# Kernel optimization log

Measured on AMD Instinct MI355X. Metric: run time of the kernel, lower is better.

## Reference

```python
import jax, jax.numpy as jnp
import numpy as np

V = 100000   # input_size == output_size (item vocab)
H = 256      # hidden_size
B = 512      # batch_size
L = 1        # num_layers


def setup_inputs() -> dict:
    key = jax.random.key(0)
    k0, k1, k2, k3, k4 = jax.random.split(key, 5)
    s = 1.0 / np.sqrt(H)  # pytorch default uniform bound scale
    return {
        "input": jax.random.randint(k0, (B,), 0, V),
        "target": jax.random.randint(k1, (B,), 0, V),
        "hidden": jnp.zeros((L, B, H), jnp.float32),
        # GRU weights, pytorch gate layout [r; z; n]
        "w_ih": jax.random.uniform(k2, (3 * H, V), jnp.float32, -s, s),
        "w_hh": jax.random.uniform(k3, (3 * H, H), jnp.float32, -s, s),
        "b_ih": jnp.zeros((3 * H,), jnp.float32),
        "b_hh": jnp.zeros((3 * H,), jnp.float32),
        # h2o linear
        "w_out": jax.random.uniform(k4, (V, H), jnp.float32, -s, s),
        "b_out": jnp.zeros((V,), jnp.float32),
    }


def reference(input, target, hidden, w_ih, w_hh, b_ih, b_hh, w_out, b_out):
    # one-hot(input) @ w_ih.T is mathematically a column gather of w_ih
    h = hidden[0]                                        # (B, H)
    gi = jnp.take(w_ih, input, axis=1).T + b_ih          # (B, 3H)
    gh = h @ w_hh.T + b_hh                               # (B, 3H)
    i_r, i_z, i_n = jnp.split(gi, 3, axis=1)
    h_r, h_z, h_n = jnp.split(gh, 3, axis=1)
    r = jax.nn.sigmoid(i_r + h_r)
    z = jax.nn.sigmoid(i_z + h_z)
    n = jnp.tanh(i_n + r * h_n)
    h_new = (1.0 - z) * n + z * h                        # (B, H)
    logit = jnp.tanh(h_new @ w_out.T + b_out)            # (B, V)
    return logit, h_new[None]                            # ((B,V), (L,B,H))
```

## Files before the change

kernel.cpp:

```cpp
#include <hip/hip_runtime.h>
#include <hip/hip_bf16.h>
#include <math.h>

#define V 100000
#define H 256
#define B 512

typedef __bf16 bf16x8 __attribute__((ext_vector_type(8)));
typedef float  f32x4  __attribute__((ext_vector_type(4)));

__device__ __forceinline__ unsigned short f32_bf16_rne(float x) {
    unsigned u = __float_as_uint(x);
    u += 0x7FFFu + ((u >> 16) & 1u);
    return (unsigned short)(u >> 16);
}
__device__ __forceinline__ float bf16u_f32(unsigned short h) {
    return __uint_as_float(((unsigned)h) << 16);
}
__device__ __forceinline__ float fast_tanh(float x) {
    float e = __builtin_exp2f(x * 2.8853900817779268f);
    return 1.f - 2.f * __builtin_amdgcn_rcpf(e + 1.f);
}

#define GLOAD_LDS16(g, l)                                                     \
    __builtin_amdgcn_global_load_lds(                                         \
        (const __attribute__((address_space(1))) void*)(g),                   \
        (__attribute__((address_space(3))) void*)(l), 16, 0, 0)

__global__ __launch_bounds__(256) void split_w_kernel(
    const float*    __restrict__ w,
    unsigned short* __restrict__ hi,
    unsigned short* __restrict__ lo)
{
    const int total4 = (V * H) / 4;
    for (int i = blockIdx.x * blockDim.x + threadIdx.x; i < total4;
         i += gridDim.x * blockDim.x) {
        const float4 x = reinterpret_cast<const float4*>(w)[i];
        const float f[4] = {x.x, x.y, x.z, x.w};
        ushort4 hv, lv;
        unsigned short* hp = &hv.x;
        unsigned short* lp = &lv.x;
        #pragma unroll
        for (int j = 0; j < 4; ++j) {
            hp[j] = f32_bf16_rne(f[j]);
            lp[j] = f32_bf16_rne(f[j] - bf16u_f32(hp[j]));
        }
        reinterpret_cast<ushort4*>(hi)[i] = hv;
        reinterpret_cast<ushort4*>(lo)[i] = lv;
    }
}

__global__ __launch_bounds__(256) void gru_cell_kernel(
    const int*   __restrict__ input,
    const float* __restrict__ hidden,
    const float* __restrict__ w_ih,
    const float* __restrict__ w_hh,
    const float* __restrict__ b_ih,
    const float* __restrict__ b_hh,
    float*       __restrict__ h_out,
    unsigned short* __restrict__ h_hi_p,
    unsigned short* __restrict__ h_lo_p)
{
    const int b = blockIdx.x;
    const int j = threadIdx.x;

    __shared__ float hs[H];
    hs[j] = hidden[b * H + j];
    __syncthreads();

    const int idx = input[b];
    float gi_r = w_ih[ j          * V + idx] + b_ih[j];
    float gi_z = w_ih[(j +     H) * V + idx] + b_ih[j + H];
    float gi_n = w_ih[(j + 2 * H) * V + idx] + b_ih[j + 2 * H];

    const float4* wr = reinterpret_cast<const float4*>(&w_hh[ j          * H]);
    const float4* wz = reinterpret_cast<const float4*>(&w_hh[(j +     H) * H]);
    const float4* wn = reinterpret_cast<const float4*>(&w_hh[(j + 2 * H) * H]);
    const float4* h4 = reinterpret_cast<const float4*>(hs);

    float ar = 0.f, az = 0.f, an = 0.f;
    #pragma unroll 8
    for (int k = 0; k < H / 4; ++k) {
        const float4 hv = h4[k];
        const float4 a  = wr[k];
        const float4 c  = wz[k];
        const float4 d  = wn[k];
        ar += a.x * hv.x + a.y * hv.y + a.z * hv.z + a.w * hv.w;
        az += c.x * hv.x + c.y * hv.y + c.z * hv.z + c.w * hv.w;
        an += d.x * hv.x + d.y * hv.y + d.z * hv.z + d.w * hv.w;
    }

    const float h_r = ar + b_hh[j];
    const float h_z = az + b_hh[j + H];
    const float h_n = an + b_hh[j + 2 * H];

    const float r = 1.f / (1.f + expf(-(gi_r + h_r)));
    const float z = 1.f / (1.f + expf(-(gi_z + h_z)));
    const float n = tanhf(gi_n + r * h_n);
    const float hprev = hs[j];

    const float val = (1.f - z) * n + z * hprev;
    h_out[b * H + j] = val;
    if (h_hi_p != nullptr) {
        const unsigned short hh = f32_bf16_rne(val);
        h_hi_p[b * H + j] = hh;
        h_lo_p[b * H + j] = f32_bf16_rne(val - bf16u_f32(hh));
    }
}

#define BM  64
#define BN  128
#define BK  64
#define NVB 782
#define NBB 8

__global__ __launch_bounds__(256) void out_gemm_lds(
    const unsigned short* __restrict__ whi_g,
    const unsigned short* __restrict__ wlo_g,
    const unsigned short* __restrict__ hhi_g,
    const unsigned short* __restrict__ hlo_g,
    const float*          __restrict__ b_out,
    float*                __restrict__ logit)
{
    __shared__ unsigned short w_hi_s[BN * BK];
    __shared__ unsigned short w_lo_s[BN * BK];
    __shared__ unsigned short h_hi_s[BM * BK];
    __shared__ unsigned short h_lo_s[BM * BK];

    const int tid  = threadIdx.x;
    const int lane = tid & 63;
    const int wid  = tid >> 6;
    const int wm   = wid >> 1;
    const int wn   = wid & 1;

    const int bid = blockIdx.x;
    const int wg  = (bid & 7) * NVB + (bid >> 3);
    const int bx  = wg & 7;
    const int by  = wg >> 3;
    const int b0  = bx * BM;
    const int v0  = by * BN;

    auto stage = [&](int k0) {
        #pragma unroll
        for (int i = 0; i < 4; ++i) {
            const int p    = i * 4096 + (wid << 10) + (lane << 4);
            const int row  = p >> 7;
            const int lb   = p & 127;
            const int swz  = lb ^ ((row & 7) << 4);
            int vg = v0 + row; if (vg > V - 1) vg = V - 1;
            const size_t gb = (size_t)vg * (H * 2) + (size_t)(k0 * 2) + swz;
            const int dst  = i * 4096 + (wid << 10);
            GLOAD_LDS16((const char*)whi_g + gb, (char*)w_hi_s + dst);
            GLOAD_LDS16((const char*)wlo_g + gb, (char*)w_lo_s + dst);
        }
        #pragma unroll
        for (int i = 0; i < 2; ++i) {
            const int p    = i * 4096 + (wid << 10) + (lane << 4);
            const int row  = p >> 7;
            const int lb   = p & 127;
            const int swz  = lb ^ ((row & 7) << 4);
            const size_t gb = (size_t)(b0 + row) * (H * 2) + (size_t)(k0 * 2) + swz;
            const int dst  = i * 4096 + (wid << 10);
            GLOAD_LDS16((const char*)hhi_g + gb, (char*)h_hi_s + dst);
            GLOAD_LDS16((const char*)hlo_g + gb, (char*)h_lo_s + dst);
        }
    };

    f32x4 acc[2][4];
    #pragma unroll
    for (int i = 0; i < 2; ++i)
        #pragma unroll
        for (int n = 0; n < 4; ++n)
            acc[i][n] = f32x4{0.f, 0.f, 0.f, 0.f};

    auto compute = [&]() {
        #pragma unroll
        for (int ks = 0; ks < 2; ++ks) {
            const int kb = ks * 64 + (lane >> 4) * 16;
            bf16x8 ah[2], al[2];
            #pragma unroll
            for (int i = 0; i < 2; ++i) {
                const int row = wm * 32 + i * 16 + (lane & 15);
                const int off = row * (BK * 2) + (kb ^ ((row & 7) << 4));
                ah[i] = *reinterpret_cast<const bf16x8*>(
                            reinterpret_cast<const char*>(h_hi_s) + off);
                al[i] = *reinterpret_cast<const bf16x8*>(
                            reinterpret_cast<const char*>(h_lo_s) + off);
            }
            #pragma unroll
            for (int n = 0; n < 4; ++n) {
                const int row = wn * 64 + n * 16 + (lane & 15);
                const int off = row * (BK * 2) + (kb ^ ((row & 7) << 4));
                const bf16x8 bh = *reinterpret_cast<const bf16x8*>(
                            reinterpret_cast<const char*>(w_hi_s) + off);
                const bf16x8 bl = *reinterpret_cast<const bf16x8*>(
                            reinterpret_cast<const char*>(w_lo_s) + off);
                #pragma unroll
                for (int i = 0; i < 2; ++i) {
                    acc[i][n] = __builtin_amdgcn_mfma_f32_16x16x32_bf16(ah[i], bh, acc[i][n], 0, 0, 0);
                    acc[i][n] = __builtin_amdgcn_mfma_f32_16x16x32_bf16(ah[i], bl, acc[i][n], 0, 0, 0);
                    acc[i][n] = __builtin_amdgcn_mfma_f32_16x16x32_bf16(al[i], bh, acc[i][n], 0, 0, 0);
                }
            }
        }
    };

    #pragma unroll
    for (int t = 0; t < 4; ++t) {
        stage(t * BK);
        __syncthreads();
        compute();
        __syncthreads();
    }

    float bias[4];
    int   cols[4];
    #pragma unroll
    for (int n = 0; n < 4; ++n) {
        const int c = v0 + wn * 64 + n * 16 + (lane & 15);
        cols[n] = c;
        bias[n] = (c < V) ? b_out[c] : 0.f;
    }
    const int rbase = b0 + wm * 32 + (lane >> 4) * 4;
    #pragma unroll
    for (int i = 0; i < 2; ++i) {
        #pragma unroll
        for (int r = 0; r < 4; ++r) {
            const int row = rbase + i * 16 + r;
            float* dst = logit + (size_t)row * V;
            #pragma unroll
            for (int n = 0; n < 4; ++n) {
                if (cols[n] < V)
                    dst[cols[n]] = fast_tanh(acc[i][n][r] + bias[n]);
            }
        }
    }
}

__global__ __launch_bounds__(256) void out_gemm_mfma_reg(
    const float* __restrict__ hnew,
    const float* __restrict__ w_out,
    const float* __restrict__ b_out,
    float*       __restrict__ logit)
{
    __shared__ unsigned short w_hi[BN * BK];
    __shared__ unsigned short w_lo[BN * BK];
    __shared__ unsigned short h_hi[BM * BK];
    __shared__ unsigned short h_lo[BM * BK];

    const int tid  = threadIdx.x;
    const int lane = tid & 63;
    const int wid  = tid >> 6;
    const int wm   = wid >> 1;
    const int wn   = wid & 1;

    const int bid = blockIdx.x;
    const int wg  = (bid & 7) * NVB + (bid >> 3);
    const int bx  = wg & 7;
    const int by  = wg >> 3;
    const int b0  = bx * BM;
    const int v0  = by * BN;

    float4 wreg[8];
    float4 hreg[4];

    auto load_chunk = [&](int k0) {
        #pragma unroll
        for (int i = 0; i < 8; ++i) {
            const int idx4 = i * 256 + tid;
            const int row  = idx4 >> 4;
            const int k4   = (idx4 & 15) << 2;
            int vg = v0 + row; if (vg > V - 1) vg = V - 1;
            wreg[i] = *reinterpret_cast<const float4*>(&w_out[(size_t)vg * H + k0 + k4]);
        }
        #pragma unroll
        for (int i = 0; i < 4; ++i) {
            const int idx4 = i * 256 + tid;
            const int row  = idx4 >> 4;
            const int k4   = (idx4 & 15) << 2;
            hreg[i] = *reinterpret_cast<const float4*>(&hnew[(b0 + row) * H + k0 + k4]);
        }
    };

    auto store_chunk = [&]() {
        #pragma unroll
        for (int i = 0; i < 8; ++i) {
            const int idx4 = i * 256 + tid;
            const int row  = idx4 >> 4;
            const int k4   = (idx4 & 15) << 2;
            const int off  = row * (BK * 2) + ((k4 * 2) ^ ((row & 7) << 4));
            const float f[4] = {wreg[i].x, wreg[i].y, wreg[i].z, wreg[i].w};
            unsigned short hv[4], lv[4];
            #pragma unroll
            for (int j = 0; j < 4; ++j) {
                hv[j] = f32_bf16_rne(f[j]);
                lv[j] = f32_bf16_rne(f[j] - bf16u_f32(hv[j]));
            }
            *reinterpret_cast<ushort4*>(reinterpret_cast<char*>(w_hi) + off) =
                make_ushort4(hv[0], hv[1], hv[2], hv[3]);
            *reinterpret_cast<ushort4*>(reinterpret_cast<char*>(w_lo) + off) =
                make_ushort4(lv[0], lv[1], lv[2], lv[3]);
        }
        #pragma unroll
        for (int i = 0; i < 4; ++i) {
            const int idx4 = i * 256 + tid;
            const int row  = idx4 >> 4;
            const int k4   = (idx4 & 15) << 2;
            const int off  = row * (BK * 2) + ((k4 * 2) ^ ((row & 7) << 4));
            const float f[4] = {hreg[i].x, hreg[i].y, hreg[i].z, hreg[i].w};
            unsigned short hv[4], lv[4];
            #pragma unroll
            for (int j = 0; j < 4; ++j) {
                hv[j] = f32_bf16_rne(f[j]);
                lv[j] = f32_bf16_rne(f[j] - bf16u_f32(hv[j]));
            }
            *reinterpret_cast<ushort4*>(reinterpret_cast<char*>(h_hi) + off) =
                make_ushort4(hv[0], hv[1], hv[2], hv[3]);
            *reinterpret_cast<ushort4*>(reinterpret_cast<char*>(h_lo) + off) =
                make_ushort4(lv[0], lv[1], lv[2], lv[3]);
        }
    };

    f32x4 acc[2][4];
    #pragma unroll
    for (int i = 0; i < 2; ++i)
        #pragma unroll
        for (int n = 0; n < 4; ++n)
            acc[i][n] = f32x4{0.f, 0.f, 0.f, 0.f};

    auto compute = [&]() {
        #pragma unroll
        for (int ks = 0; ks < 2; ++ks) {
            const int kb = ks * 64 + (lane >> 4) * 16;
            bf16x8 ah[2], al[2];
            #pragma unroll
            for (int i = 0; i < 2; ++i) {
                const int row = wm * 32 + i * 16 + (lane & 15);
                const int off = row * (BK * 2) + (kb ^ ((row & 7) << 4));
                ah[i] = *reinterpret_cast<const bf16x8*>(
                            reinterpret_cast<const char*>(h_hi) + off);
                al[i] = *reinterpret_cast<const bf16x8*>(
                            reinterpret_cast<const char*>(h_lo) + off);
            }
            #pragma unroll
            for (int n = 0; n < 4; ++n) {
                const int row = wn * 64 + n * 16 + (lane & 15);
                const int off = row * (BK * 2) + (kb ^ ((row & 7) << 4));
                const bf16x8 bh = *reinterpret_cast<const bf16x8*>(
                            reinterpret_cast<const char*>(w_hi) + off);
                const bf16x8 bl = *reinterpret_cast<const bf16x8*>(
                            reinterpret_cast<const char*>(w_lo) + off);
                #pragma unroll
                for (int i = 0; i < 2; ++i) {
                    acc[i][n] = __builtin_amdgcn_mfma_f32_16x16x32_bf16(ah[i], bh, acc[i][n], 0, 0, 0);
                    acc[i][n] = __builtin_amdgcn_mfma_f32_16x16x32_bf16(ah[i], bl, acc[i][n], 0, 0, 0);
                    acc[i][n] = __builtin_amdgcn_mfma_f32_16x16x32_bf16(al[i], bh, acc[i][n], 0, 0, 0);
                }
            }
        }
    };

    load_chunk(0);
    store_chunk();
    __syncthreads();
    for (int t = 0; t < 4; ++t) {
        if (t < 3) load_chunk((t + 1) * BK);
        compute();
        __syncthreads();
        if (t < 3) { store_chunk(); __syncthreads(); }
    }

    float bias[4];
    int   cols[4];
    #pragma unroll
    for (int n = 0; n < 4; ++n) {
        const int c = v0 + wn * 64 + n * 16 + (lane & 15);
        cols[n] = c;
        bias[n] = (c < V) ? b_out[c] : 0.f;
    }
    const int rbase = b0 + wm * 32 + (lane >> 4) * 4;
    #pragma unroll
    for (int i = 0; i < 2; ++i) {
        #pragma unroll
        for (int r = 0; r < 4; ++r) {
            const int row = rbase + i * 16 + r;
            float* dst = logit + (size_t)row * V;
            #pragma unroll
            for (int n = 0; n < 4; ++n) {
                if (cols[n] < V)
                    dst[cols[n]] = tanhf(acc[i][n][r] + bias[n]);
            }
        }
    }
}

extern "C" void kernel_launch(void* const* d_in, const int* in_sizes, int n_in,
                              void* d_out, int out_size, void* d_ws, size_t ws_size,
                              hipStream_t stream) {
    const int*   input  = (const int*)  d_in[0];
    const float* hidden = (const float*)d_in[2];
    const float* w_ih   = (const float*)d_in[3];
    const float* w_hh   = (const float*)d_in[4];
    const float* b_ih   = (const float*)d_in[5];
    const float* b_hh   = (const float*)d_in[6];
    const float* w_out  = (const float*)d_in[7];
    const float* b_out  = (const float*)d_in[8];

    float* out   = (float*)d_out;
    float* logit = out;
    float* h_new = out + (size_t)B * V;

    const size_t nw = (size_t)V * H;
    const size_t nh = (size_t)B * H;
    const size_t needed = (2 * nw + 2 * nh) * sizeof(unsigned short);

    if (ws_size >= needed) {
        unsigned short* whi = (unsigned short*)d_ws;
        unsigned short* wlo = whi + nw;
        unsigned short* hhi = wlo + nw;
        unsigned short* hlo = hhi + nh;

        split_w_kernel<<<2048, 256, 0, stream>>>(w_out, whi, wlo);
        gru_cell_kernel<<<B, 256, 0, stream>>>(input, hidden, w_ih, w_hh,
                                               b_ih, b_hh, h_new, hhi, hlo);
        out_gemm_lds<<<NVB * NBB, 256, 0, stream>>>(whi, wlo, hhi, hlo,
                                                    b_out, logit);
    } else {
        gru_cell_kernel<<<B, 256, 0, stream>>>(input, hidden, w_ih, w_hh,
                                               b_ih, b_hh, h_new,
                                               nullptr, nullptr);
        out_gemm_mfma_reg<<<NVB * NBB, 256, 0, stream>>>(h_new, w_out,
                                                         b_out, logit);
    }
}
```

Measured before the change: 253.4 us.

## Fuse weight bf16 hi/lo split into output GEMM with full-batch tiles

Removes the separate split_w kernel and its workspace round-trip: the output GEMM now loads fp32 w_out directly into registers, splits it into bf16 hi/lo and writes the halves to LDS, prefetching the next K slice while computing. Each block covers all 512 batch rows for a 64-column vocab tile, so each weight element is read once. The hidden-state hi/lo fragments are read straight from global memory instead of LDS. The cost is a large register footprint (32 accumulator tiles per wave), fewer blocks, and uncached-by-LDS global reads of h on every k-step.

```diff
diff --git a/kernel.cpp b/kernel.cpp
--- a/kernel.cpp
+++ b/kernel.cpp
@@ -20,34 +20,6 @@
 __device__ __forceinline__ float fast_tanh(float x) {
     float e = __builtin_exp2f(x * 2.8853900817779268f);
     return 1.f - 2.f * __builtin_amdgcn_rcpf(e + 1.f);
-}
-
-#define GLOAD_LDS16(g, l)                                                     \
-    __builtin_amdgcn_global_load_lds(                                         \
-        (const __attribute__((address_space(1))) void*)(g),                   \
-        (__attribute__((address_space(3))) void*)(l), 16, 0, 0)
-
-__global__ __launch_bounds__(256) void split_w_kernel(
-    const float*    __restrict__ w,
-    unsigned short* __restrict__ hi,
-    unsigned short* __restrict__ lo)
-{
-    const int total4 = (V * H) / 4;
-    for (int i = blockIdx.x * blockDim.x + threadIdx.x; i < total4;
-         i += gridDim.x * blockDim.x) {
-        const float4 x = reinterpret_cast<const float4*>(w)[i];
-        const float f[4] = {x.x, x.y, x.z, x.w};
-        ushort4 hv, lv;
-        unsigned short* hp = &hv.x;
-        unsigned short* lp = &lv.x;
-        #pragma unroll
-        for (int j = 0; j < 4; ++j) {
-            hp[j] = f32_bf16_rne(f[j]);
-            lp[j] = f32_bf16_rne(f[j] - bf16u_f32(hp[j]));
-        }
-        reinterpret_cast<ushort4*>(hi)[i] = hv;
-        reinterpret_cast<ushort4*>(lo)[i] = lv;
-    }
 }
 
 __global__ __launch_bounds__(256) void gru_cell_kernel(
@@ -108,108 +80,106 @@
     }
 }
 
-#define BM  64
-#define BN  128
+#define VT  64
 #define BK  64
-#define NVB 782
-#define NBB 8
-
-__global__ __launch_bounds__(256) void out_gemm_lds(
-    const unsigned short* __restrict__ whi_g,
-    const unsigned short* __restrict__ wlo_g,
+#define NVB2 1563
+
+__global__ __launch_bounds__(256, 2) void out_gemm_fused(
+    const float*          __restrict__ w_out,
     const unsigned short* __restrict__ hhi_g,
     const unsigned short* __restrict__ hlo_g,
     const float*          __restrict__ b_out,
     float*                __restrict__ logit)
 {
-    __shared__ unsigned short w_hi_s[BN * BK];
-    __shared__ unsigned short w_lo_s[BN * BK];
-    __shared__ unsigned short h_hi_s[BM * BK];
-    __shared__ unsigned short h_lo_s[BM * BK];
+    __shared__ unsigned short w_hi_s[VT * BK];
+    __shared__ unsigned short w_lo_s[VT * BK];
 
     const int tid  = threadIdx.x;
     const int lane = tid & 63;
     const int wid  = tid >> 6;
-    const int wm   = wid >> 1;
-    const int wn   = wid & 1;
-
-    const int bid = blockIdx.x;
-    const int wg  = (bid & 7) * NVB + (bid >> 3);
-    const int bx  = wg & 7;
-    const int by  = wg >> 3;
-    const int b0  = bx * BM;
-    const int v0  = by * BN;
-
-    auto stage = [&](int k0) {
+    const int v0   = blockIdx.x * VT;
+
+    float4 wreg[4];
+
+    auto load_w = [&](int k0) {
         #pragma unroll
         for (int i = 0; i < 4; ++i) {
-            const int p    = i * 4096 + (wid << 10) + (lane << 4);
-            const int row  = p >> 7;
-            const int lb   = p & 127;
-            const int swz  = lb ^ ((row & 7) << 4);
+            const int u   = i * 256 + tid;
+            const int row = u >> 4;
+            const int k4  = (u & 15) << 2;
             int vg = v0 + row; if (vg > V - 1) vg = V - 1;
-            const size_t gb = (size_t)vg * (H * 2) + (size_t)(k0 * 2) + swz;
-            const int dst  = i * 4096 + (wid << 10);
-            GLOAD_LDS16((const char*)whi_g + gb, (char*)w_hi_s + dst);
-            GLOAD_LDS16((const char*)wlo_g + gb, (char*)w_lo_s + dst);
-        }
-        #pragma unroll
-        for (int i = 0; i < 2; ++i) {
-            const int p    = i * 4096 + (wid << 10) + (lane << 4);
-            const int row  = p >> 7;
-            const int lb   = p & 127;
-            const int swz  = lb ^ ((row & 7) << 4);
-            const size_t gb = (size_t)(b0 + row) * (H * 2) + (size_t)(k0 * 2) + swz;
-            const int dst  = i * 4096 + (wid << 10);
-            GLOAD_LDS16((const char*)hhi_g + gb, (char*)h_hi_s + dst);
-            GLOAD_LDS16((const char*)hlo_g + gb, (char*)h_lo_s + dst);
-        }
-    };
-
-    f32x4 acc[2][4];
-    #pragma unroll
-    for (int i = 0; i < 2; ++i)
+            wreg[i] = *reinterpret_cast<const float4*>(&w_out[(size_t)vg * H + k0 + k4]);
+        }
+    };
+
+    auto store_w = [&]() {
+        #pragma unroll
+        for (int i = 0; i < 4; ++i) {
+            const int u   = i * 256 + tid;
+            const int row = u >> 4;
+            const int k4  = (u & 15) << 2;
+            const int off = row * (BK * 2) + ((k4 * 2) ^ ((row & 7) << 4));
+            const float f[4] = {wreg[i].x, wreg[i].y, wreg[i].z, wreg[i].w};
+            unsigned short hv[4], lv[4];
+            #pragma unroll
+            for (int j = 0; j < 4; ++j) {
+                hv[j] = f32_bf16_rne(f[j]);
+                lv[j] = f32_bf16_rne(f[j] - bf16u_f32(hv[j]));
+            }
+            *reinterpret_cast<ushort4*>(reinterpret_cast<char*>(w_hi_s) + off) =
+                make_ushort4(hv[0], hv[1], hv[2], hv[3]);
+            *reinterpret_cast<ushort4*>(reinterpret_cast<char*>(w_lo_s) + off) =
+                make_ushort4(lv[0], lv[1], lv[2], lv[3]);
+        }
+    };
+
+    f32x4 acc[8][4];
+    #pragma unroll
+    for (int m = 0; m < 8; ++m)
         #pragma unroll
         for (int n = 0; n < 4; ++n)
-            acc[i][n] = f32x4{0.f, 0.f, 0.f, 0.f};
-
-    auto compute = [&]() {
+            acc[m][n] = f32x4{0.f, 0.f, 0.f, 0.f};
+
+    auto compute = [&](int t) {
         #pragma unroll
         for (int ks = 0; ks < 2; ++ks) {
             const int kb = ks * 64 + (lane >> 4) * 16;
-            bf16x8 ah[2], al[2];
-            #pragma unroll
-            for (int i = 0; i < 2; ++i) {
-                const int row = wm * 32 + i * 16 + (lane & 15);
+            bf16x8 bh[4], bl[4];
+            #pragma unroll
+            for (int n = 0; n < 4; ++n) {
+                const int row = n * 16 + (lane & 15);
                 const int off = row * (BK * 2) + (kb ^ ((row & 7) << 4));
-                ah[i] = *reinterpret_cast<const bf16x8*>(
-                            reinterpret_cast<const char*>(h_hi_s) + off);
-                al[i] = *reinterpret_cast<const bf16x8*>(
-                            reinterpret_cast<const char*>(h_lo_s) + off);
-            }
-            #pragma unroll
-            for (int n = 0; n < 4; ++n) {
-                const int row = wn * 64 + n * 16 + (lane & 15);
-                const int off = row * (BK * 2) + (kb ^ ((row & 7) << 4));
-                const bf16x8 bh = *reinterpret_cast<const bf16x8*>(
+                bh[n] = *reinterpret_cast<const bf16x8*>(
                             reinterpret_cast<const char*>(w_hi_s) + off);
-                const bf16x8 bl = *reinterpret_cast<const bf16x8*>(
+                bl[n] = *reinterpret_cast<const bf16x8*>(
                             reinterpret_cast<const char*>(w_lo_s) + off);
+            }
+            const size_t hb = ((size_t)(wid * 128 + (lane & 15)) * H
+                               + t * BK + ks * 32 + (lane >> 4) * 8) * 2;
+            #pragma unroll
+            for (int m = 0; m < 8; ++m) {
+                const size_t ho = hb + (size_t)(m * 16) * (H * 2);
+                const bf16x8 ah = *reinterpret_cast<const bf16x8*>(
+                            reinterpret_cast<const char*>(hhi_g) + ho);
+                const bf16x8 al = *reinterpret_cast<const bf16x8*>(
+                            reinterpret_cast<const char*>(hlo_g) + ho);
                 #pragma unroll
-                for (int i = 0; i < 2; ++i) {
-                    acc[i][n] = __builtin_amdgcn_mfma_f32_16x16x32_bf16(ah[i], bh, acc[i][n], 0, 0, 0);
-                    acc[i][n] = __builtin_amdgcn_mfma_f32_16x16x32_bf16(ah[i], bl, acc[i][n], 0, 0, 0);
-                    acc[i][n] = __builtin_amdgcn_mfma_f32_16x16x32_bf16(al[i], bh, acc[i][n], 0, 0, 0);
+                for (int n = 0; n < 4; ++n) {
+                    acc[m][n] = __builtin_amdgcn_mfma_f32_16x16x32_bf16(ah, bh[n], acc[m][n], 0, 0, 0);
+                    acc[m][n] = __builtin_amdgcn_mfma_f32_16x16x32_bf16(ah, bl[n], acc[m][n], 0, 0, 0);
+                    acc[m][n] = __builtin_amdgcn_mfma_f32_16x16x32_bf16(al, bh[n], acc[m][n], 0, 0, 0);
                 }
             }
         }
     };
 
+    load_w(0);
     #pragma unroll
     for (int t = 0; t < 4; ++t) {
-        stage(t * BK);
+        store_w();
         __syncthreads();
-        compute();
+        if (t < 3) load_w((t + 1) * BK);
+        compute(t);
         __syncthreads();
     }
 
@@ -217,25 +187,30 @@
     int   cols[4];
     #pragma unroll
     for (int n = 0; n < 4; ++n) {
-        const int c = v0 + wn * 64 + n * 16 + (lane & 15);
+        const int c = v0 + n * 16 + (lane & 15);
         cols[n] = c;
         bias[n] = (c < V) ? b_out[c] : 0.f;
     }
-    const int rbase = b0 + wm * 32 + (lane >> 4) * 4;
-    #pragma unroll
-    for (int i = 0; i < 2; ++i) {
+    const int rbase = wid * 128 + (lane >> 4) * 4;
+    #pragma unroll
+    for (int m = 0; m < 8; ++m) {
         #pragma unroll
         for (int r = 0; r < 4; ++r) {
-            const int row = rbase + i * 16 + r;
+            const int row = rbase + m * 16 + r;
             float* dst = logit + (size_t)row * V;
             #pragma unroll
             for (int n = 0; n < 4; ++n) {
                 if (cols[n] < V)
-                    dst[cols[n]] = fast_tanh(acc[i][n][r] + bias[n]);
-            }
-        }
-    }
-}
+                    dst[cols[n]] = fast_tanh(acc[m][n][r] + bias[n]);
+            }
+        }
+    }
+}
+
+#define BM  64
+#define BN  128
+#define NVB 782
+#define NBB 8
 
 __global__ __launch_bounds__(256) void out_gemm_mfma_reg(
     const float* __restrict__ hnew,
@@ -410,21 +385,16 @@
     float* logit = out;
     float* h_new = out + (size_t)B * V;
 
-    const size_t nw = (size_t)V * H;
     const size_t nh = (size_t)B * H;
-    const size_t needed = (2 * nw + 2 * nh) * sizeof(unsigned short);
+    const size_t needed = 2 * nh * sizeof(unsigned short);
 
     if (ws_size >= needed) {
-        unsigned short* whi = (unsigned short*)d_ws;
-        unsigned short* wlo = whi + nw;
-        unsigned short* hhi = wlo + nw;
+        unsigned short* hhi = (unsigned short*)d_ws;
         unsigned short* hlo = hhi + nh;
 
-        split_w_kernel<<<2048, 256, 0, stream>>>(w_out, whi, wlo);
         gru_cell_kernel<<<B, 256, 0, stream>>>(input, hidden, w_ih, w_hh,
                                                b_ih, b_hh, h_new, hhi, hlo);
-        out_gemm_lds<<<NVB * NBB, 256, 0, stream>>>(whi, wlo, hhi, hlo,
-                                                    b_out, logit);
+        out_gemm_fused<<<NVB2, 256, 0, stream>>>(w_out, hhi, hlo, b_out, logit);
     } else {
         gru_cell_kernel<<<B, 256, 0, stream>>>(input, hidden, w_ih, w_hh,
                                                b_ih, b_hh, h_new,
```

New measurement: 304.2 us. 1.2x slower.
